# Optimization experiments

Measured on AMD Instinct MI355X. Metric: run time of the kernel, lower is better.

Reference implementation:

```python
import jax, jax.numpy as jnp
import numpy as np

N0, N1, N2 = 100000, 50000, 25000
E0, E1 = 400000, 200000
H1, D1 = 4, 64   # layer0: 4 heads x 64
H2, D2 = 1, 64   # layer1: 1 head  x 64
SLOPE = 0.2      # DGL GATConv leaky_relu negative_slope


def gat_conv(h_src, h_dst, src, dst, W, attn_l, attn_r, bias, n_dst, heads, d):
    # linear projection (shared between src and dst, as in DGL GATConv)
    f_src = (h_src @ W).reshape(-1, heads, d)   # (N_src, H, D)
    f_dst = (h_dst @ W).reshape(-1, heads, d)   # (N_dst, H, D)
    el = jnp.einsum('nhd,hd->nh', f_src, attn_l)  # (N_src, H)
    er = jnp.einsum('nhd,hd->nh', f_dst, attn_r)  # (N_dst, H)
    e = jax.nn.leaky_relu(el[src] + er[dst], SLOPE)  # (E, H)
    # edge-softmax over incoming edges of each dst node (numerically stable)
    m = jax.ops.segment_max(e, dst, num_segments=n_dst)      # (N_dst, H)
    ee = jnp.exp(e - m[dst])
    s = jax.ops.segment_sum(ee, dst, num_segments=n_dst)
    alpha = ee / s[dst]                                      # (E, H)
    msg = f_src[src] * alpha[:, :, None]                     # (E, H, D)
    out = jax.ops.segment_sum(msg, dst, num_segments=n_dst)  # (N_dst, H, D)
    return out + bias.reshape(1, heads, d)


def setup_inputs() -> dict:
    key = jax.random.key(0)
    ks = jax.random.split(key, 12)
    return {
        'x': jax.random.normal(ks[0], (N0, 256), jnp.float32),
        'e0_src': jax.random.randint(ks[1], (E0,), 0, N0, jnp.int32),
        'e0_dst': jax.random.randint(ks[2], (E0,), 0, N1, jnp.int32),
        'e1_src': jax.random.randint(ks[3], (E1,), 0, N1, jnp.int32),
        'e1_dst': jax.random.randint(ks[4], (E1,), 0, N2, jnp.int32),
        'W1': jax.random.normal(ks[5], (256, H1 * D1), jnp.float32) * 0.06,
        'al1': jax.random.normal(ks[6], (H1, D1), jnp.float32) * 0.1,
        'ar1': jax.random.normal(ks[7], (H1, D1), jnp.float32) * 0.1,
        'b1': jnp.zeros((H1 * D1,), jnp.float32),
        'W2': jax.random.normal(ks[8], (H1 * D1, H2 * D2), jnp.float32) * 0.06,
        'al2': jax.random.normal(ks[9], (H2, D2), jnp.float32) * 0.1,
        'ar2': jax.random.normal(ks[10], (H2, D2), jnp.float32) * 0.1,
        'b2': jnp.zeros((H2 * D2,), jnp.float32),
    }


def reference(x, e0_src, e0_dst, e1_src, e1_dst,
              W1, al1, ar1, b1, W2, al2, ar2, b2):
    # layer 0: block 100k src -> 50k dst; dst nodes are a prefix of src nodes
    h = gat_conv(x, x[:N1], e0_src, e0_dst, W1, al1, ar1, b1, N1, H1, D1)
    h = jax.nn.relu(h).reshape(N1, H1 * D1)   # activation + flatten(1); dropout is identity at eval
    # layer 1 (final): single head, no activation, flatten
    h = gat_conv(h, h[:N2], e1_src, e1_dst, W2, al2, ar2, b2, N2, H2, D2)
    return h.reshape(N2, H2 * D2)
```

## Files before the change

### kernel.cpp

```cpp
#include <hip/hip_runtime.h>
#include <cstddef>
#include <cstdint>

constexpr int cN0 = 100000, cN1 = 50000, cN2 = 25000;
constexpr int cE0 = 400000, cE1 = 200000;
constexpr float SLOPE = 0.2f;

typedef short short8  __attribute__((ext_vector_type(8)));
typedef short short4v __attribute__((ext_vector_type(4)));
typedef float f32x4   __attribute__((ext_vector_type(4)));

__device__ __forceinline__ unsigned short f2bf(float x) {
    union { float f; uint32_t u; } c; c.f = x;
    uint32_t u = c.u + 0x7FFFu + ((c.u >> 16) & 1u);
    return (unsigned short)(u >> 16);
}
__device__ __forceinline__ float bf2f(uint32_t u) {
    union { uint32_t u; float f; } c; c.u = u << 16; return c.f;
}
__device__ __forceinline__ float lrelu(float x) { return x >= 0.f ? x : SLOPE * x; }

__device__ __forceinline__ uint32_t cvtpk(float lo, float hi) {
    uint32_t r;
    asm("v_cvt_pk_bf16_f32 %0, %1, %2" : "=v"(r) : "v"(lo), "v"(hi));
    return r;
}

__device__ __forceinline__ void gload_lds16(const void* g, void* l) {
    __builtin_amdgcn_global_load_lds(
        (const __attribute__((address_space(1))) unsigned int*)g,
        (__attribute__((address_space(3))) unsigned int*)l, 16, 0, 0);
}


__global__ void hist2_kernel(const int* __restrict__ d0, const int* __restrict__ d1,
                             int* __restrict__ cnt0, int* __restrict__ cnt1) {
    int i = blockIdx.x * blockDim.x + threadIdx.x;
    if (i < cE0) atomicAdd(&cnt0[d0[i]], 1);
    int j = i - cE0;
    if (j >= 0 && j < cE1) atomicAdd(&cnt1[d1[j]], 1);
}

__global__ __launch_bounds__(256) void chunk_sum2_kernel(const int* __restrict__ cnt0, int n0,
                                                         const int* __restrict__ cnt1, int n1,
                                                         int* __restrict__ bsum0, int* __restrict__ bsum1,
                                                         int nblk1) {
    const int* cnt = blockIdx.y ? cnt1 : cnt0;
    int n = blockIdx.y ? n1 : n0;
    int* bsum = blockIdx.y ? bsum1 : bsum0;
    if (blockIdx.y && (int)blockIdx.x >= nblk1) return;
    int i = blockIdx.x * 256 + threadIdx.x;
    int v = (i < n) ? cnt[i] : 0;
    #pragma unroll
    for (int o = 32; o; o >>= 1) v += __shfl_xor(v, o);
    __shared__ int ws[4];
    if ((threadIdx.x & 63) == 0) ws[threadIdx.x >> 6] = v;
    __syncthreads();
    if (threadIdx.x == 0) bsum[blockIdx.x] = ws[0] + ws[1] + ws[2] + ws[3];
}

__device__ __forceinline__ int block_exscan(int v, int& total) {
    int lane = threadIdx.x & 63, w = threadIdx.x >> 6;
    int x = v;
    #pragma unroll
    for (int o = 1; o < 64; o <<= 1) { int t = __shfl_up(x, o); if (lane >= o) x += t; }
    __shared__ int ws[4];
    if (lane == 63) ws[w] = x;
    __syncthreads();
    int add = 0;
    #pragma unroll
    for (int i = 0; i < 4; ++i) if (i < w) add += ws[i];
    total = ws[0] + ws[1] + ws[2] + ws[3];
    return add + x - v;
}

__global__ __launch_bounds__(256) void top_scan2_kernel(const int* __restrict__ bsum0, int nblk0,
                                                        const int* __restrict__ bsum1, int nblk1,
                                                        int* __restrict__ boff0, int* __restrict__ boff1,
                                                        int* __restrict__ tot0, int* __restrict__ tot1) {
    int i = threadIdx.x;
    int tot;
    int v = (i < nblk0) ? bsum0[i] : 0;
    int e = block_exscan(v, tot);
    if (i < nblk0) boff0[i] = e;
    if (i == 0) *tot0 = tot;
    __syncthreads();
    v = (i < nblk1) ? bsum1[i] : 0;
    e = block_exscan(v, tot);
    if (i < nblk1) boff1[i] = e;
    if (i == 0) *tot1 = tot;
}

__global__ __launch_bounds__(256) void chunk_scan2_kernel(const int* __restrict__ cnt0, int n0,
                                                          const int* __restrict__ cnt1, int n1,
                                                          const int* __restrict__ boff0, const int* __restrict__ boff1,
                                                          int* __restrict__ offs0, int* __restrict__ cursor0,
                                                          int* __restrict__ offs1, int* __restrict__ cursor1,
                                                          int nblk1) {
    const int* cnt = blockIdx.y ? cnt1 : cnt0;
    const int* boff = blockIdx.y ? boff1 : boff0;
    int* offs = blockIdx.y ? offs1 : offs0;
    int* cursor = blockIdx.y ? cursor1 : cursor0;
    int n = blockIdx.y ? n1 : n0;
    if (blockIdx.y && (int)blockIdx.x >= nblk1) return;
    int i = blockIdx.x * 256 + threadIdx.x;
    int v = (i < n) ? cnt[i] : 0;
    int tot; int e = block_exscan(v, tot) + boff[blockIdx.x];
    if (i < n) { offs[i] = e; cursor[i] = e; }
}

__global__ void scatter2_kernel(const int* __restrict__ s0, const int* __restrict__ d0,
                                const int* __restrict__ s1, const int* __restrict__ d1,
                                int* __restrict__ cursor0, int* __restrict__ srcidx0,
                                int* __restrict__ cursor1, int* __restrict__ srcidx1) {
    int i = blockIdx.x * blockDim.x + threadIdx.x;
    if (i < cE0) { int p = atomicAdd(&cursor0[d0[i]], 1); srcidx0[p] = s0[i]; }
    int j = i - cE0;
    if (j >= 0 && j < cE1) { int p = atomicAdd(&cursor1[d1[j]], 1); srcidx1[p] = s1[j]; }
}

__global__ __launch_bounds__(256) void bf16_transpose2_kernel(const float* __restrict__ W1,
                                                              const float* __restrict__ W2,
                                                              short* __restrict__ bt1,
                                                              short* __restrict__ bt2) {
    int i = blockIdx.x * 256 + threadIdx.x;
    if (i < 256 * 256) {
        int k = i >> 8, n = i & 255;
        bt1[(size_t)n * 256 + k] = (short)f2bf(W1[i]);
    } else {
        int j = i - 256 * 256;
        if (j < 256 * 64) {
            int k = j >> 6, n = j & 63;
            bt2[(size_t)n * 256 + k] = (short)f2bf(W2[j]);
        }
    }
}

__global__ __launch_bounds__(512, 4) void gemm0_deep(
    const float* __restrict__ A, const short* __restrict__ BT,
    unsigned short* __restrict__ C,
    const float* __restrict__ al, const float* __restrict__ ar,
    float* __restrict__ el, float* __restrict__ er,
    int M, int erN)
{
    constexpr int T = 8;
    constexpr int nh = 4;
    __shared__ float Asm[2][128 * 32];
    __shared__ short Bsm[2][256 * 32];

    const int tid = threadIdx.x;
    const int w = tid >> 6;
    const int lane = tid & 63;
    const int ln = lane & 15;
    const int kg = lane >> 4;
    const int wr = w >> 2;
    const int wc = w & 3;
    const int m0 = blockIdx.x * 128;

    f32x4 acc[4][4];
    #pragma unroll
    for (int mi = 0; mi < 4; ++mi)
        #pragma unroll
        for (int ni = 0; ni < 4; ++ni)
            #pragma unroll
            for (int j = 0; j < 4; ++j) acc[mi][ni][j] = 0.f;

    auto stageA = [&](int k0, int b) {
        #pragma unroll
        for (int q = 0; q < 2; ++q) {
            int ci = w + q * 8;
            int r = ci * 8 + (lane >> 3);
            int cl = (lane & 7) ^ (r & 7);
            int gr = m0 + r; if (gr >= M) gr = M - 1;
            gload_lds16(&A[(size_t)gr * 256 + k0 + cl * 4], &Asm[b][ci * 256]);
        }
    };
    auto stageB = [&](int k0, int b) {
        #pragma unroll
        for (int q = 0; q < 2; ++q) {
            int ci = w + q * 8;
            int r = ci * 16 + (lane >> 2);
            int cl = (lane & 3) ^ ((r >> 1) & 3);
            gload_lds16(&BT[(size_t)r * 256 + k0 + cl * 8], &Bsm[b][ci * 512]);
        }
    };

    stageA(0, 0); stageB(0, 0);
    __syncthreads();

    const int swa = ln & 7;
    const int p0base = 2 * kg;
    const int pb = kg ^ ((ln >> 1) & 3);

    int cur = 0;
    #pragma unroll
    for (int t = 0; t < T; ++t) {
        if (t + 1 < T) { stageA((t + 1) * 32, cur ^ 1); stageB((t + 1) * 32, cur ^ 1); }

        short8 af[4];
        {
            int pA = p0base ^ swa;
            #pragma unroll
            for (int mi = 0; mi < 4; ++mi) {
                int r = wr * 64 + mi * 16 + ln;
                const f32x4 q0 = *(const f32x4*)&Asm[cur][r * 32 + pA * 4];
                const f32x4 q1 = *(const f32x4*)&Asm[cur][r * 32 + (pA ^ 1) * 4];
                union { uint32_t u[4]; short8 s; } cv;
                cv.u[0] = cvtpk(q0[0], q0[1]);
                cv.u[1] = cvtpk(q0[2], q0[3]);
                cv.u[2] = cvtpk(q1[0], q1[1]);
                cv.u[3] = cvtpk(q1[2], q1[3]);
                af[mi] = cv.s;
            }
        }
        #pragma unroll
        for (int ni = 0; ni < 4; ++ni) {
            int rB = wc * 64 + ni * 16 + ln;
            short8 bf = *(const short8*)&Bsm[cur][rB * 32 + pb * 8];
            #pragma unroll
            for (int mi = 0; mi < 4; ++mi)
                acc[mi][ni] = __builtin_amdgcn_mfma_f32_16x16x32_bf16(af[mi], bf, acc[mi][ni], 0, 0, 0);
        }
        __syncthreads();
        cur ^= 1;
    }

    const int h = wc;
    float alv[4], arv[4];
    #pragma unroll
    for (int ni = 0; ni < 4; ++ni) {
        alv[ni] = al[h * 64 + ni * 16 + ln];
        arv[ni] = ar[h * 64 + ni * 16 + ln];
    }
    #pragma unroll
    for (int mi = 0; mi < 4; ++mi) {
        float pl[4] = {0, 0, 0, 0}, pr[4] = {0, 0, 0, 0};
        #pragma unroll
        for (int ni = 0; ni < 4; ++ni)
            #pragma unroll
            for (int j = 0; j < 4; ++j) {
                float v = acc[mi][ni][j];
                pl[j] += v * alv[ni];
                pr[j] += v * arv[ni];
            }
        #pragma unroll
        for (int j = 0; j < 4; ++j)
            #pragma unroll
            for (int o = 1; o < 16; o <<= 1) {
                pl[j] += __shfl_xor(pl[j], o);
                pr[j] += __shfl_xor(pr[j], o);
            }
        #pragma unroll
        for (int j = 0; j < 4; ++j) {
            int row = m0 + wr * 64 + mi * 16 + kg * 4 + j;
            if (row < M) {
                #pragma unroll
                for (int ni = 0; ni < 4; ++ni)
                    C[(size_t)row * 256 + wc * 64 + ni * 16 + ln] = f2bf(acc[mi][ni][j]);
                if (ln == 0) {
                    el[row * nh + h] = pl[j];
                    if (row < erN) er[row * nh + h] = pr[j];
                }
            }
        }
    }
}

template<int BM, int BN, int WR, int WC>
__global__ __launch_bounds__(256) void gemm_bf16_fused(
    const unsigned short* __restrict__ A, const short* __restrict__ BT,
    unsigned short* __restrict__ C,
    const float* __restrict__ al, const float* __restrict__ ar,
    float* __restrict__ el, float* __restrict__ er,
    int M, int K, int nh, int erN)
{
    constexpr int BK = 32;
    constexpr int PITCH = BK + 8;
    constexpr int MI = BM / WR / 16;
    constexpr int NI = BN / WC / 16;
    constexpr int AITB = BM * 4 / 256;
    constexpr int BIT  = BN * 4 / 256;

    __shared__ short As[BM * PITCH];
    __shared__ short Bs[BN * PITCH];

    const int tid = threadIdx.x;
    const int w = tid >> 6;
    const int lane = tid & 63;
    const int ln = lane & 15;
    const int kg = lane >> 4;
    const int wr = w / WC;
    const int wc = w % WC;
    const int m0 = blockIdx.x * BM;
    const int n0 = blockIdx.y * BN;
    const int N = nh * 64;

    f32x4 acc[MI][NI];
    #pragma unroll
    for (int mi = 0; mi < MI; ++mi)
        #pragma unroll
        for (int ni = 0; ni < NI; ++ni)
            #pragma unroll
            for (int j = 0; j < 4; ++j) acc[mi][ni][j] = 0.f;

    short8 aregb[AITB];
    short8 breg[BIT];

    auto loadA = [&](int k0) {
        #pragma unroll
        for (int p = 0; p < AITB; ++p) {
            int slot = tid + p * 256;
            int r = slot >> 2;
            int kq = (slot & 3) * 8;
            int gr = m0 + r;
            short8 v = {};
            if (gr < M) v = *(const short8*)&A[(size_t)gr * K + k0 + kq];
            aregb[p] = v;
        }
    };
    auto loadB = [&](int k0) {
        #pragma unroll
        for (int p = 0; p < BIT; ++p) {
            int slot = tid + p * 256;
            int r = slot >> 2;
            int kq = (slot & 3) * 8;
            breg[p] = *(const short8*)&BT[(size_t)(n0 + r) * K + k0 + kq];
        }
    };
    auto writeLDS = [&]() {
        #pragma unroll
        for (int p = 0; p < AITB; ++p) {
            int slot = tid + p * 256;
            int r = slot >> 2;
            int kq = (slot & 3) * 8;
            *(short8*)&As[r * PITCH + kq] = aregb[p];
        }
        #pragma unroll
        for (int p = 0; p < BIT; ++p) {
            int slot = tid + p * 256;
            int r = slot >> 2;
            int kq = (slot & 3) * 8;
            *(short8*)&Bs[r * PITCH + kq] = breg[p];
        }
    };

    loadA(0); loadB(0);
    const int T = K / BK;
    for (int t = 0; t < T; ++t) {
        writeLDS();
        __syncthreads();
        if (t + 1 < T) { loadA((t + 1) * BK); loadB((t + 1) * BK); }
        short8 af[MI], bf[NI];
        #pragma unroll
        for (int mi = 0; mi < MI; ++mi)
            af[mi] = *(const short8*)&As[(wr * MI * 16 + mi * 16 + ln) * PITCH + kg * 8];
        #pragma unroll
        for (int ni = 0; ni < NI; ++ni)
            bf[ni] = *(const short8*)&Bs[(wc * NI * 16 + ni * 16 + ln) * PITCH + kg * 8];
        #pragma unroll
        for (int mi = 0; mi < MI; ++mi)
            #pragma unroll
            for (int ni = 0; ni < NI; ++ni)
                acc[mi][ni] = __builtin_amdgcn_mfma_f32_16x16x32_bf16(af[mi], bf[ni], acc[mi][ni], 0, 0, 0);
        __syncthreads();
    }

    const int h = (n0 + wc * NI * 16) >> 6;
    float alv[NI], arv[NI];
    #pragma unroll
    for (int ni = 0; ni < NI; ++ni) {
        alv[ni] = al[h * 64 + ni * 16 + ln];
        arv[ni] = ar[h * 64 + ni * 16 + ln];
    }
    #pragma unroll
    for (int mi = 0; mi < MI; ++mi) {
        float pl[4] = {0, 0, 0, 0}, pr[4] = {0, 0, 0, 0};
        #pragma unroll
        for (int ni = 0; ni < NI; ++ni)
            #pragma unroll
            for (int j = 0; j < 4; ++j) {
                float v = acc[mi][ni][j];
                pl[j] += v * alv[ni];
                pr[j] += v * arv[ni];
            }
        #pragma unroll
        for (int j = 0; j < 4; ++j)
            #pragma unroll
            for (int o = 1; o < 16; o <<= 1) {
                pl[j] += __shfl_xor(pl[j], o);
                pr[j] += __shfl_xor(pr[j], o);
            }
        #pragma unroll
        for (int j = 0; j < 4; ++j) {
            int row = m0 + wr * MI * 16 + mi * 16 + kg * 4 + j;
            if (row < M) {
                #pragma unroll
                for (int ni = 0; ni < NI; ++ni)
                    C[(size_t)row * N + n0 + wc * NI * 16 + ni * 16 + ln] = f2bf(acc[mi][ni][j]);
                if (ln == 0) {
                    el[row * nh + h] = pl[j];
                    if (row < erN) er[row * nh + h] = pr[j];
                }
            }
        }
    }
}


__global__ __launch_bounds__(256) void agg0_kernel(const int* __restrict__ offs,
                                                   const int* __restrict__ srcidx,
                                                   const float* __restrict__ el,
                                                   const float* __restrict__ er,
                                                   const unsigned short* __restrict__ fb,
                                                   const float* __restrict__ bias,
                                                   unsigned short* __restrict__ h1b) {
    int w = threadIdx.x >> 6, lane = threadIdx.x & 63;
    int n = blockIdx.x * 4 + w;
    if (n >= cN1) return;
    int beg = offs[n], end = offs[n + 1];

    int h4 = lane & 3, sub = lane >> 2;
    float erA = er[n * 4 + h4];
    float m = -1e30f, s = 0.f;
    for (int i = beg + sub; i < end; i += 16) {
        int sv = srcidx[i];
        float e = lrelu(el[sv * 4 + h4] + erA);
        if (e > m) { s = s * __expf(m - e) + 1.f; m = e; }
        else s += __expf(e - m);
    }
    #pragma unroll
    for (int o = 4; o < 64; o <<= 1) {
        float m2 = __shfl_xor(m, o), s2 = __shfl_xor(s, o);
        float M = fmaxf(m, m2);
        s = s * __expf(m - M) + s2 * __expf(m2 - M);
        m = M;
    }
    float inv = (s > 0.f) ? 1.f / s : 0.f;

    int half = lane >> 5, lcol = lane & 31;
    int hB = lcol >> 3;
    float mB = __shfl(m, hB);
    float invB = __shfl(inv, hB);
    float erB = __shfl(erA, hB);

    float a[8] = {};
    for (int i = beg + half; i < end; i += 2) {
        int sv = srcidx[i];
        float e = lrelu(el[sv * 4 + hB] + erB);
        float p = __expf(e - mB) * invB;
        uint4 v = *(const uint4*)&fb[(size_t)sv * 256 + lcol * 8];
        a[0] = fmaf(bf2f(v.x & 0xffffu), p, a[0]);
        a[1] = fmaf(bf2f(v.x >> 16),     p, a[1]);
        a[2] = fmaf(bf2f(v.y & 0xffffu), p, a[2]);
        a[3] = fmaf(bf2f(v.y >> 16),     p, a[3]);
        a[4] = fmaf(bf2f(v.z & 0xffffu), p, a[4]);
        a[5] = fmaf(bf2f(v.z >> 16),     p, a[5]);
        a[6] = fmaf(bf2f(v.w & 0xffffu), p, a[6]);
        a[7] = fmaf(bf2f(v.w >> 16),     p, a[7]);
    }
    #pragma unroll
    for (int j = 0; j < 8; ++j) a[j] += __shfl_xor(a[j], 32);
    if (half == 0) {
        short8 r;
        #pragma unroll
        for (int j = 0; j < 8; ++j) {
            float o = a[j] + bias[lcol * 8 + j];
            r[j] = (short)f2bf(o > 0.f ? o : 0.f);
        }
        *(short8*)&h1b[(size_t)n * 256 + lcol * 8] = r;
    }
}

__global__ __launch_bounds__(256) void agg1_kernel(const int* __restrict__ offs,
                                                   const int* __restrict__ srcidx,
                                                   const float* __restrict__ el,
                                                   const float* __restrict__ er,
                                                   const unsigned short* __restrict__ f2b,
                                                   const float* __restrict__ bias,
                                                   float* __restrict__ out) {
    int w = threadIdx.x >> 6, lane = threadIdx.x & 63;
    int n = blockIdx.x * 4 + w;
    if (n >= cN2) return;
    int beg = offs[n], end = offs[n + 1];
    float ern = er[n];

    float m = -1e30f, s = 0.f;
    for (int i = beg + lane; i < end; i += 64) {
        float e = lrelu(el[srcidx[i]] + ern);
        if (e > m) { s = s * __expf(m - e) + 1.f; m = e; }
        else s += __expf(e - m);
    }
    #pragma unroll
    for (int o = 1; o < 64; o <<= 1) {
        float m2 = __shfl_xor(m, o), s2 = __shfl_xor(s, o);
        float M = fmaxf(m, m2);
        s = s * __expf(m - M) + s2 * __expf(m2 - M);
        m = M;
    }
    float inv = (s > 0.f) ? 1.f / s : 0.f;

    int q = lane >> 4, lcol = lane & 15;
    float a[4] = {};
    for (int i = beg + q; i < end; i += 4) {
        int sv = srcidx[i];
        float e = lrelu(el[sv] + ern);
        float p = __expf(e - m) * inv;
        uint2 v = *(const uint2*)&f2b[(size_t)sv * 64 + lcol * 4];
        a[0] = fmaf(bf2f(v.x & 0xffffu), p, a[0]);
        a[1] = fmaf(bf2f(v.x >> 16),     p, a[1]);
        a[2] = fmaf(bf2f(v.y & 0xffffu), p, a[2]);
        a[3] = fmaf(bf2f(v.y >> 16),     p, a[3]);
    }
    #pragma unroll
    for (int o = 16; o < 64; o <<= 1)
        #pragma unroll
        for (int j = 0; j < 4; ++j) a[j] += __shfl_xor(a[j], o);
    if (q == 0) {
        float4 b4 = *(const float4*)&bias[lcol * 4];
        float4 r = make_float4(a[0] + b4.x, a[1] + b4.y, a[2] + b4.z, a[3] + b4.w);
        *(float4*)&out[(size_t)n * 64 + lcol * 4] = r;
    }
}


extern "C" void kernel_launch(void* const* d_in, const int* in_sizes, int n_in,
                              void* d_out, int out_size, void* d_ws, size_t ws_size,
                              hipStream_t stream) {
    const float* x      = (const float*)d_in[0];
    const int*   e0_src = (const int*)d_in[1];
    const int*   e0_dst = (const int*)d_in[2];
    const int*   e1_src = (const int*)d_in[3];
    const int*   e1_dst = (const int*)d_in[4];
    const float* W1     = (const float*)d_in[5];
    const float* al1    = (const float*)d_in[6];
    const float* ar1    = (const float*)d_in[7];
    const float* b1     = (const float*)d_in[8];
    const float* W2     = (const float*)d_in[9];
    const float* al2    = (const float*)d_in[10];
    const float* ar2    = (const float*)d_in[11];
    const float* b2     = (const float*)d_in[12];
    float* out = (float*)d_out;

    char* ws = (char*)d_ws;
    size_t off = 0;
    auto alloc = [&](size_t bytes) -> void* {
        void* p = ws + off;
        off = (off + bytes + 255) & ~(size_t)255;
        return p;
    };
    unsigned short* fb  = (unsigned short*)alloc((size_t)cN0 * 256 * 2);
    unsigned short* h1b = (unsigned short*)alloc((size_t)cN1 * 256 * 2);
    unsigned short* f2b = (unsigned short*)alloc((size_t)cN1 * 64 * 2);
    float* el0  = (float*)alloc((size_t)cN0 * 4 * 4);
    float* er0  = (float*)alloc((size_t)cN1 * 4 * 4);
    float* el2  = (float*)alloc((size_t)cN1 * 4);
    float* er2  = (float*)alloc((size_t)cN2 * 4);
    short* bt1  = (short*)alloc((size_t)256 * 256 * 2);
    short* bt2  = (short*)alloc((size_t)64 * 256 * 2);
    int* cntB    = (int*)alloc((size_t)(cN1 + cN2) * 4);
    int* cnt0    = cntB;
    int* cnt1    = cntB + cN1;
    int* offs0   = (int*)alloc((size_t)(cN1 + 1) * 4);
    int* cursor0 = (int*)alloc((size_t)cN1 * 4);
    int* srcidx0 = (int*)alloc((size_t)cE0 * 4);
    int* offs1   = (int*)alloc((size_t)(cN2 + 1) * 4);
    int* cursor1 = (int*)alloc((size_t)cN2 * 4);
    int* srcidx1 = (int*)alloc((size_t)cE1 * 4);
    int* bsum0   = (int*)alloc(256 * 4);
    int* boff0   = (int*)alloc(256 * 4);
    int* bsum1   = (int*)alloc(256 * 4);
    int* boff1   = (int*)alloc(256 * 4);
    (void)ws_size; (void)n_in; (void)in_sizes; (void)out_size;

    const int nblk0 = (cN1 + 255) / 256;
    const int nblk1 = (cN2 + 255) / 256;

    hipMemsetAsync(cntB, 0, (size_t)(cN1 + cN2) * 4, stream);
    hist2_kernel<<<(cE0 + cE1 + 255) / 256, 256, 0, stream>>>(e0_dst, e1_dst, cnt0, cnt1);
    chunk_sum2_kernel<<<dim3(nblk0, 2), 256, 0, stream>>>(cnt0, cN1, cnt1, cN2, bsum0, bsum1, nblk1);
    top_scan2_kernel<<<1, 256, 0, stream>>>(bsum0, nblk0, bsum1, nblk1, boff0, boff1,
                                            offs0 + cN1, offs1 + cN2);
    chunk_scan2_kernel<<<dim3(nblk0, 2), 256, 0, stream>>>(cnt0, cN1, cnt1, cN2, boff0, boff1,
                                                           offs0, cursor0, offs1, cursor1, nblk1);
    scatter2_kernel<<<(cE0 + cE1 + 255) / 256, 256, 0, stream>>>(e0_src, e0_dst, e1_src, e1_dst,
                                                                 cursor0, srcidx0, cursor1, srcidx1);
    bf16_transpose2_kernel<<<(256 * 256 + 256 * 64 + 255) / 256, 256, 0, stream>>>(W1, W2, bt1, bt2);

    gemm0_deep<<<(cN0 + 127) / 128, 512, 0, stream>>>(x, bt1, fb, al1, ar1, el0, er0, cN0, cN1);
    agg0_kernel<<<(cN1 + 3) / 4, 256, 0, stream>>>(offs0, srcidx0, el0, er0, fb, b1, h1b);

    gemm_bf16_fused<128, 64, 4, 1><<<dim3((cN1 + 127) / 128, 1), 256, 0, stream>>>(
        h1b, bt2, f2b, al2, ar2, el2, er2, cN1, 256, 1, cN2);
    agg1_kernel<<<(cN2 + 3) / 4, 256, 0, stream>>>(offs1, srcidx1, el2, er2, f2b, b2, out);
}
```

Before: 184.3 us.

## Keep full bf16 weight matrix resident in LDS and stream A from registers

The first-layer GEMM now loads the whole 256x256 bf16 weight matrix into 128KB of shared memory once per block. Each wave computes 32 rows across all 256 columns, with A fetched straight from global memory into registers and double-buffered there. This removes the per-k-step LDS staging of A and B and the block-wide barriers inside the k loop. In exchange it uses much more LDS and many accumulator registers (2x16 f32x4 per lane) at launch bounds (512,2). The global A loads are uncoalesced strided reads, and the large LDS footprint likely limits occupancy to one block per CU.

```diff
diff --git a/kernel.cpp b/kernel.cpp
--- a/kernel.cpp
+++ b/kernel.cpp
@@ -136,130 +136,116 @@
     }
 }
 
-__global__ __launch_bounds__(512, 4) void gemm0_deep(
+__global__ __launch_bounds__(512, 2) void gemm0_breg(
     const float* __restrict__ A, const short* __restrict__ BT,
     unsigned short* __restrict__ C,
     const float* __restrict__ al, const float* __restrict__ ar,
     float* __restrict__ el, float* __restrict__ er,
     int M, int erN)
 {
-    constexpr int T = 8;
-    constexpr int nh = 4;
-    __shared__ float Asm[2][128 * 32];
-    __shared__ short Bsm[2][256 * 32];
+    __shared__ short Bs[256 * 256];
 
     const int tid = threadIdx.x;
     const int w = tid >> 6;
     const int lane = tid & 63;
     const int ln = lane & 15;
     const int kg = lane >> 4;
-    const int wr = w >> 2;
-    const int wc = w & 3;
-    const int m0 = blockIdx.x * 128;
-
-    f32x4 acc[4][4];
-    #pragma unroll
-    for (int mi = 0; mi < 4; ++mi)
-        #pragma unroll
-        for (int ni = 0; ni < 4; ++ni)
+    const int m0 = blockIdx.x * 256;
+
+    #pragma unroll
+    for (int i = 0; i < 16; ++i) {
+        int seg = 2 * (i * 8 + w);
+        int r = seg + (lane >> 5);
+        int c = (lane & 31) ^ (r & 7);
+        gload_lds16(&BT[(size_t)r * 256 + c * 8], &Bs[(size_t)seg * 256]);
+    }
+
+    f32x4 acc[2][16];
+    #pragma unroll
+    for (int mi = 0; mi < 2; ++mi)
+        #pragma unroll
+        for (int ni = 0; ni < 16; ++ni)
             #pragma unroll
             for (int j = 0; j < 4; ++j) acc[mi][ni][j] = 0.f;
 
-    auto stageA = [&](int k0, int b) {
-        #pragma unroll
-        for (int q = 0; q < 2; ++q) {
-            int ci = w + q * 8;
-            int r = ci * 8 + (lane >> 3);
-            int cl = (lane & 7) ^ (r & 7);
-            int gr = m0 + r; if (gr >= M) gr = M - 1;
-            gload_lds16(&A[(size_t)gr * 256 + k0 + cl * 4], &Asm[b][ci * 256]);
-        }
+    int r0 = m0 + w * 32 + ln;      if (r0 >= M) r0 = M - 1;
+    int r1 = m0 + w * 32 + 16 + ln; if (r1 >= M) r1 = M - 1;
+    const float* ap0 = A + (size_t)r0 * 256 + kg * 8;
+    const float* ap1 = A + (size_t)r1 * 256 + kg * 8;
+
+    float4 pa[2][2][2];
+    auto loadA = [&](int kt, int buf) {
+        pa[buf][0][0] = *(const float4*)(ap0 + kt * 32);
+        pa[buf][0][1] = *(const float4*)(ap0 + kt * 32 + 4);
+        pa[buf][1][0] = *(const float4*)(ap1 + kt * 32);
+        pa[buf][1][1] = *(const float4*)(ap1 + kt * 32 + 4);
     };
-    auto stageB = [&](int k0, int b) {
-        #pragma unroll
-        for (int q = 0; q < 2; ++q) {
-            int ci = w + q * 8;
-            int r = ci * 16 + (lane >> 2);
-            int cl = (lane & 3) ^ ((r >> 1) & 3);
-            gload_lds16(&BT[(size_t)r * 256 + k0 + cl * 8], &Bsm[b][ci * 512]);
-        }
-    };
-
-    stageA(0, 0); stageB(0, 0);
+
+    loadA(0, 0);
     __syncthreads();
 
-    const int swa = ln & 7;
-    const int p0base = 2 * kg;
-    const int pb = kg ^ ((ln >> 1) & 3);
-
-    int cur = 0;
-    #pragma unroll
-    for (int t = 0; t < T; ++t) {
-        if (t + 1 < T) { stageA((t + 1) * 32, cur ^ 1); stageB((t + 1) * 32, cur ^ 1); }
-
-        short8 af[4];
-        {
-            int pA = p0base ^ swa;
-            #pragma unroll
-            for (int mi = 0; mi < 4; ++mi) {
-                int r = wr * 64 + mi * 16 + ln;
-                const f32x4 q0 = *(const f32x4*)&Asm[cur][r * 32 + pA * 4];
-                const f32x4 q1 = *(const f32x4*)&Asm[cur][r * 32 + (pA ^ 1) * 4];
-                union { uint32_t u[4]; short8 s; } cv;
-                cv.u[0] = cvtpk(q0[0], q0[1]);
-                cv.u[1] = cvtpk(q0[2], q0[3]);
-                cv.u[2] = cvtpk(q1[0], q1[1]);
-                cv.u[3] = cvtpk(q1[2], q1[3]);
-                af[mi] = cv.s;
+    const int swb = ln & 7;
+    #pragma unroll
+    for (int kt = 0; kt < 8; ++kt) {
+        const int buf = kt & 1;
+        if (kt + 1 < 8) loadA(kt + 1, buf ^ 1);
+        short8 af[2];
+        #pragma unroll
+        for (int mi = 0; mi < 2; ++mi) {
+            const float4 p0 = pa[buf][mi][0];
+            const float4 p1 = pa[buf][mi][1];
+            union { uint32_t u[4]; short8 s; } cv;
+            cv.u[0] = cvtpk(p0.x, p0.y);
+            cv.u[1] = cvtpk(p0.z, p0.w);
+            cv.u[2] = cvtpk(p1.x, p1.y);
+            cv.u[3] = cvtpk(p1.z, p1.w);
+            af[mi] = cv.s;
+        }
+        #pragma unroll
+        for (int ni = 0; ni < 16; ++ni) {
+            int row = ni * 16 + ln;
+            int pc = (kt * 4 + kg) ^ swb;
+            short8 bf = *(const short8*)&Bs[row * 256 + pc * 8];
+            acc[0][ni] = __builtin_amdgcn_mfma_f32_16x16x32_bf16(af[0], bf, acc[0][ni], 0, 0, 0);
+            acc[1][ni] = __builtin_amdgcn_mfma_f32_16x16x32_bf16(af[1], bf, acc[1][ni], 0, 0, 0);
+        }
+    }
+
+    float alv[16], arv[16];
+    #pragma unroll
+    for (int ni = 0; ni < 16; ++ni) {
+        alv[ni] = al[ni * 16 + ln];
+        arv[ni] = ar[ni * 16 + ln];
+    }
+    #pragma unroll
+    for (int mi = 0; mi < 2; ++mi) {
+        #pragma unroll
+        for (int j = 0; j < 4; ++j) {
+            float pl[4] = {0, 0, 0, 0}, pr[4] = {0, 0, 0, 0};
+            #pragma unroll
+            for (int ni = 0; ni < 16; ++ni) {
+                float v = acc[mi][ni][j];
+                pl[ni >> 2] += v * alv[ni];
+                pr[ni >> 2] += v * arv[ni];
             }
-        }
-        #pragma unroll
-        for (int ni = 0; ni < 4; ++ni) {
-            int rB = wc * 64 + ni * 16 + ln;
-            short8 bf = *(const short8*)&Bsm[cur][rB * 32 + pb * 8];
-            #pragma unroll
-            for (int mi = 0; mi < 4; ++mi)
-                acc[mi][ni] = __builtin_amdgcn_mfma_f32_16x16x32_bf16(af[mi], bf, acc[mi][ni], 0, 0, 0);
-        }
-        __syncthreads();
-        cur ^= 1;
-    }
-
-    const int h = wc;
-    float alv[4], arv[4];
-    #pragma unroll
-    for (int ni = 0; ni < 4; ++ni) {
-        alv[ni] = al[h * 64 + ni * 16 + ln];
-        arv[ni] = ar[h * 64 + ni * 16 + ln];
-    }
-    #pragma unroll
-    for (int mi = 0; mi < 4; ++mi) {
-        float pl[4] = {0, 0, 0, 0}, pr[4] = {0, 0, 0, 0};
-        #pragma unroll
-        for (int ni = 0; ni < 4; ++ni)
-            #pragma unroll
-            for (int j = 0; j < 4; ++j) {
-                float v = acc[mi][ni][j];
-                pl[j] += v * alv[ni];
-                pr[j] += v * arv[ni];
-            }
-        #pragma unroll
-        for (int j = 0; j < 4; ++j)
-            #pragma unroll
-            for (int o = 1; o < 16; o <<= 1) {
-                pl[j] += __shfl_xor(pl[j], o);
-                pr[j] += __shfl_xor(pr[j], o);
-            }
-        #pragma unroll
-        for (int j = 0; j < 4; ++j) {
-            int row = m0 + wr * 64 + mi * 16 + kg * 4 + j;
+            #pragma unroll
+            for (int h = 0; h < 4; ++h)
+                #pragma unroll
+                for (int o = 1; o < 16; o <<= 1) {
+                    pl[h] += __shfl_xor(pl[h], o);
+                    pr[h] += __shfl_xor(pr[h], o);
+                }
+            int row = m0 + w * 32 + mi * 16 + kg * 4 + j;
             if (row < M) {
                 #pragma unroll
-                for (int ni = 0; ni < 4; ++ni)
-                    C[(size_t)row * 256 + wc * 64 + ni * 16 + ln] = f2bf(acc[mi][ni][j]);
+                for (int ni = 0; ni < 16; ++ni)
+                    C[(size_t)row * 256 + ni * 16 + ln] = f2bf(acc[mi][ni][j]);
                 if (ln == 0) {
-                    el[row * nh + h] = pl[j];
-                    if (row < erN) er[row * nh + h] = pr[j];
+                    #pragma unroll
+                    for (int h = 0; h < 4; ++h) {
+                        el[row * 4 + h] = pl[h];
+                        if (row < erN) er[row * 4 + h] = pr[h];
+                    }
                 }
             }
         }
@@ -586,7 +572,7 @@
                                                                  cursor0, srcidx0, cursor1, srcidx1);
     bf16_transpose2_kernel<<<(256 * 256 + 256 * 64 + 255) / 256, 256, 0, stream>>>(W1, W2, bt1, bt2);
 
-    gemm0_deep<<<(cN0 + 127) / 128, 512, 0, stream>>>(x, bt1, fb, al1, ar1, el0, er0, cN0, cN1);
+    gemm0_breg<<<(cN0 + 255) / 256, 512, 0, stream>>>(x, bt1, fb, al1, ar1, el0, er0, cN0, cN1);
     agg0_kernel<<<(cN1 + 3) / 4, 256, 0, stream>>>(offs0, srcidx0, el0, er0, fb, b1, h1b);
 
     gemm_bf16_fused<128, 64, 4, 1><<<dim3((cN1 + 127) / 128, 1), 256, 0, stream>>>(
```

New measurement: 189.6 us. 1.03x slower.
